# Kernel optimization log

Hardware: AMD Instinct MI355X
Metric: run time of the kernel (lower is better)

Reference implementation:

```python
import jax, jax.numpy as jnp
import numpy as np
import itertools

N_INPUTS = 6
N_TERMS = 4
# static rule index table [R, n_inputs], R = n_terms ** n_inputs = 4096
RULE_IDX = np.array(list(itertools.product(range(N_TERMS), repeat=N_INPUTS)), dtype=np.int32)


def setup_inputs() -> dict:
    key = jax.random.key(0)
    k1, k2, k3, k4 = jax.random.split(key, 4)
    B = 32768
    x = jax.random.normal(k1, (B, N_INPUTS), dtype=jnp.float32)
    centers = jax.random.normal(k2, (N_INPUTS, N_TERMS), dtype=jnp.float32)
    sigmas = jax.random.uniform(k3, (N_INPUTS, N_TERMS), dtype=jnp.float32, minval=0.5, maxval=1.5)
    consequents = jax.random.normal(k4, (N_TERMS ** N_INPUTS, N_INPUTS + 1), dtype=jnp.float32)
    return {"x": x, "centers": centers, "sigmas": sigmas, "consequents": consequents}


def reference(x, centers, sigmas, consequents):
    # Gaussian memberships: mu[b, i, t]
    s = jnp.abs(sigmas) + 1e-6                          # [I, T]
    mu = jnp.exp(-((x[:, :, None] - centers[None]) ** 2) / (2.0 * s[None] ** 2))  # [B, I, T]
    # rule firing strengths: product over inputs of selected terms
    idx = jnp.asarray(RULE_IDX.T)                       # [I, R]
    mu_sel = jnp.take_along_axis(mu, idx[None], axis=2)  # [B, I, R]
    w = jnp.prod(mu_sel, axis=1)                        # [B, R]
    w_norm = w / (jnp.sum(w, axis=1, keepdims=True) + 1e-8)
    # consequent outputs: f[b, r] = [x, 1] @ consequents[r]
    x_aug = jnp.concatenate([x, jnp.ones((x.shape[0], 1), dtype=x.dtype)], axis=1)  # [B, I+1]
    f = x_aug @ consequents.T                           # [B, R]
    return jnp.sum(w_norm * f, axis=1, keepdims=True)   # [B, 1]
```

## Files before the change

kernel.cpp:

```cpp
#include <hip/hip_runtime.h>


typedef __attribute__((ext_vector_type(8))) short bf16x8;
typedef __attribute__((ext_vector_type(4))) float f32x4;

#define THREADS 512
#define BPB     128
#define C2T_ROW_W 260
#define C2T_WORDS (64 * C2T_ROW_W)
#define PH_STR  66
#define PTT_STR 132
#define LDS_BYTES ((C2T_WORDS + BPB * PH_STR + 64 * PTT_STR) * 4)

__device__ __forceinline__ unsigned int bf16rne(float f) {
    unsigned int u = __float_as_uint(f);
    u += 0x7fffu + ((u >> 16) & 1u);
    return u >> 16;
}

__global__ void anfis_prep(const float* __restrict__ cons, unsigned int* __restrict__ ws) {
    int idx = blockIdx.x * blockDim.x + threadIdx.x;
    if (idx >= 64 * 256) return;
    int n = idx >> 8;
    int w = idx & 255;
    int c0 = w * 2;
    unsigned int h0 = 0, h1 = 0;
    int l = c0 >> 3, j = c0 & 7;
    if (j < 7) h0 = bf16rne(cons[(n * 64 + l) * 7 + j]);
    l = (c0 + 1) >> 3; j = (c0 + 1) & 7;
    if (j < 7) h1 = bf16rne(cons[(n * 64 + l) * 7 + j]);
    ws[idx] = h0 | (h1 << 16);
}

extern __shared__ unsigned int smem[];

__launch_bounds__(THREADS, 1)
__global__ void anfis_mfma(const float* __restrict__ x,
                           const float* __restrict__ centers,
                           const float* __restrict__ sigmas,
                           const unsigned int* __restrict__ wsC,
                           float* __restrict__ out, int B) {
    unsigned int* C2T = smem;
    float* PH  = (float*)(smem + C2T_WORDS);
    float* PTT = PH + BPB * PH_STR;

    const int tid  = threadIdx.x;
    const int lane = tid & 63;
    const int wv   = tid >> 6;
    const long blockbase = (long)blockIdx.x * BPB;

    for (int i = tid; i < C2T_WORDS; i += THREADS) {
        int n  = i / C2T_ROW_W;
        int ww = i - n * C2T_ROW_W;
        C2T[i] = (ww < 256) ? wsC[(n << 8) + ww] : 0u;
    }

    {
        const int d0 = (lane >> 4) & 3, d1 = (lane >> 2) & 3, d2 = lane & 3;
        float cen[6], inv[6];
        const int t6[6] = {d0, d1, d2, d0, d1, d2};
#pragma unroll
        for (int i = 0; i < 6; ++i) {
            cen[i] = centers[i * 4 + t6[i]];
            float s = fabsf(sigmas[i * 4 + t6[i]]) + 1e-6f;
            inv[i] = 0.5f / (s * s);
        }
#pragma unroll 2
        for (int g = 0; g < 16; ++g) {
            int bl = wv * 16 + g;
            long b = blockbase + bl;
            if (b >= B) b = B - 1;
            float m[6];
#pragma unroll
            for (int i = 0; i < 6; ++i) {
                float d = x[b * 6 + i] - cen[i];
                m[i] = __expf(-d * d * inv[i]);
            }
            PH[bl * PH_STR + lane]  = m[0] * m[1] * m[2];
            PTT[lane * PTT_STR + bl] = m[3] * m[4] * m[5];
        }
    }
    __syncthreads();

    const int t = lane & 15, q = lane >> 4;
    const int m0 = wv * 16;

    float xa[8];
    {
        long bm = blockbase + m0 + t;
        if (bm >= B) bm = B - 1;
#pragma unroll
        for (int j = 0; j < 6; ++j) xa[j] = x[bm * 6 + j];
        xa[6] = 1.f;
        xa[7] = 0.f;
    }

    union U4 { unsigned int u[4]; bf16x8 v; };
    U4 B4;
    B4.u[0] = B4.u[1] = B4.u[2] = 0u;
    B4.u[3] = (t == 0) ? 0x00003f80u : 0u;

    f32x4 Dn[4], D4;
#pragma unroll
    for (int nt = 0; nt < 4; ++nt) Dn[nt] = (f32x4){0.f, 0.f, 0.f, 0.f};
    D4 = (f32x4){0.f, 0.f, 0.f, 0.f};

    const unsigned short* C2Ts = (const unsigned short*)C2T;

#pragma unroll 2
    for (int kt = 0; kt < 16; ++kt) {
        float ptv = PTT[(kt * 4 + q) * PTT_STR + m0 + t];
        U4 Ah, Al;
#pragma unroll
        for (int jp = 0; jp < 4; ++jp) {
            float u0 = ptv * xa[2 * jp];
            float u1 = ptv * xa[2 * jp + 1];
            unsigned int b0 = __float_as_uint(u0), b1 = __float_as_uint(u1);
            unsigned int t0 = b0 & 0xffff0000u, t1 = b1 & 0xffff0000u;
            float l0 = u0 - __uint_as_float(t0);
            float l1 = u1 - __uint_as_float(t1);
            Ah.u[jp] = (b0 >> 16) | t1;
            Al.u[jp] = (__float_as_uint(l0) >> 16) | (__float_as_uint(l1) & 0xffff0000u);
        }
#pragma unroll
        for (int nt = 0; nt < 4; ++nt) {
            bf16x8 Bf = *(const bf16x8*)&C2Ts[(nt * 16 + t) * 520 + kt * 32 + q * 8];
            Dn[nt] = __builtin_amdgcn_mfma_f32_16x16x32_bf16(Ah.v, Bf, Dn[nt], 0, 0, 0);
            Dn[nt] = __builtin_amdgcn_mfma_f32_16x16x32_bf16(Al.v, Bf, Dn[nt], 0, 0, 0);
        }
        D4 = __builtin_amdgcn_mfma_f32_16x16x32_bf16(Ah.v, B4.v, D4, 0, 0, 0);
        D4 = __builtin_amdgcn_mfma_f32_16x16x32_bf16(Al.v, B4.v, D4, 0, 0, 0);
    }

    float Pn[4] = {0.f, 0.f, 0.f, 0.f};
    float Ps[4] = {0.f, 0.f, 0.f, 0.f};
    float Pd[4];
#pragma unroll
    for (int r = 0; r < 4; ++r) Pd[r] = D4[r];
#pragma unroll
    for (int nt = 0; nt < 4; ++nt)
#pragma unroll
        for (int r = 0; r < 4; ++r) {
            float phv = PH[(m0 + q * 4 + r) * PH_STR + nt * 16 + t];
            Pn[r] = fmaf(phv, Dn[nt][r], Pn[r]);
            Ps[r] += phv;
        }
#pragma unroll
    for (int off = 1; off < 16; off <<= 1)
#pragma unroll
        for (int r = 0; r < 4; ++r) {
            Pn[r] += __shfl_xor(Pn[r], off);
            Ps[r] += __shfl_xor(Ps[r], off);
            Pd[r] += __shfl_xor(Pd[r], off);
        }
    if (t == 0) {
        long bo = blockbase + m0 + q * 4;
        float o[4];
#pragma unroll
        for (int r = 0; r < 4; ++r) o[r] = Pn[r] / (Ps[r] * Pd[r] + 1e-8f);
        if (bo + 3 < B) {
            *(float4*)&out[bo] = make_float4(o[0], o[1], o[2], o[3]);
        } else {
#pragma unroll
            for (int r = 0; r < 4; ++r)
                if (bo + r < B) out[bo + r] = o[r];
        }
    }
}

extern "C" void kernel_launch(void* const* d_in, const int* in_sizes, int n_in,
                              void* d_out, int out_size, void* d_ws, size_t ws_size,
                              hipStream_t stream) {
    const float* x       = (const float*)d_in[0];
    const float* centers = (const float*)d_in[1];
    const float* sigmas  = (const float*)d_in[2];
    const float* cons    = (const float*)d_in[3];
    float* out = (float*)d_out;

    int B = in_sizes[0] / 6;
    unsigned int* wsC = (unsigned int*)d_ws;

    static int attr_set = 0;
    hipFuncSetAttribute(reinterpret_cast<const void*>(anfis_mfma),
                        hipFuncAttributeMaxDynamicSharedMemorySize, LDS_BYTES);
    (void)attr_set;

    anfis_prep<<<64, 256, 0, stream>>>(cons, wsC);
    int blocks = (B + BPB - 1) / BPB;
    anfis_mfma<<<blocks, THREADS, LDS_BYTES, stream>>>(x, centers, sigmas, wsC,
                                                       out, B);
}
```

Measured before the change: 80.91 us.

## Read bf16 consequents from global per wave instead of staging in LDS

The prep kernel now packs each rule's 7 consequents as one uint4 of bf16. The MFMA loop loads these packed B fragments directly from global memory, which should stay cache-resident, instead of every block first copying the whole table into LDS. Blocks shrink to 256 threads and 64 rows with 4 blocks per CU allowed. Each wave stages only its own x rows and membership partials in static shared memory, so the block-wide barrier is removed. This trades the per-block LDS fill and low occupancy for repeated global/L2 loads inside the k-loop, and it drops the tail bounds handling on x loads.

Measured after the change: 69.82 us. -13.7%, faster.

```diff
diff --git a/kernel.cpp b/kernel.cpp
--- a/kernel.cpp
+++ b/kernel.cpp
@@ -4,13 +4,10 @@
 typedef __attribute__((ext_vector_type(8))) short bf16x8;
 typedef __attribute__((ext_vector_type(4))) float f32x4;
 
-#define THREADS 512
-#define BPB     128
-#define C2T_ROW_W 260
-#define C2T_WORDS (64 * C2T_ROW_W)
+#define THREADS 256
+#define BPB     64
 #define PH_STR  66
-#define PTT_STR 132
-#define LDS_BYTES ((C2T_WORDS + BPB * PH_STR + 64 * PTT_STR) * 4)
+#define PTT_STR 65
 
 __device__ __forceinline__ unsigned int bf16rne(float f) {
     unsigned int u = __float_as_uint(f);
@@ -18,82 +15,73 @@
     return u >> 16;
 }
 
-__global__ void anfis_prep(const float* __restrict__ cons, unsigned int* __restrict__ ws) {
-    int idx = blockIdx.x * blockDim.x + threadIdx.x;
-    if (idx >= 64 * 256) return;
-    int n = idx >> 8;
-    int w = idx & 255;
-    int c0 = w * 2;
-    unsigned int h0 = 0, h1 = 0;
-    int l = c0 >> 3, j = c0 & 7;
-    if (j < 7) h0 = bf16rne(cons[(n * 64 + l) * 7 + j]);
-    l = (c0 + 1) >> 3; j = (c0 + 1) & 7;
-    if (j < 7) h1 = bf16rne(cons[(n * 64 + l) * 7 + j]);
-    ws[idx] = h0 | (h1 << 16);
+__global__ void anfis_prep(const float* __restrict__ cons, uint4* __restrict__ ws) {
+    int id = blockIdx.x * blockDim.x + threadIdx.x;
+    if (id >= 4096) return;
+    int l = id >> 6, n = id & 63;
+    const float* src = cons + (n * 64 + l) * 7;
+    unsigned int h[8];
+#pragma unroll
+    for (int j = 0; j < 7; ++j) h[j] = bf16rne(src[j]);
+    h[7] = 0;
+    uint4 v;
+    v.x = h[0] | (h[1] << 16);
+    v.y = h[2] | (h[3] << 16);
+    v.z = h[4] | (h[5] << 16);
+    v.w = h[6] | (h[7] << 16);
+    ws[id] = v;
 }
 
-extern __shared__ unsigned int smem[];
-
-__launch_bounds__(THREADS, 1)
+__launch_bounds__(THREADS, 4)
 __global__ void anfis_mfma(const float* __restrict__ x,
                            const float* __restrict__ centers,
                            const float* __restrict__ sigmas,
-                           const unsigned int* __restrict__ wsC,
+                           const uint4* __restrict__ wsC,
                            float* __restrict__ out, int B) {
-    unsigned int* C2T = smem;
-    float* PH  = (float*)(smem + C2T_WORDS);
-    float* PTT = PH + BPB * PH_STR;
+    __shared__ float  PH[BPB * PH_STR];
+    __shared__ float  PTT[64 * PTT_STR];
+    __shared__ float4 xs4[BPB * 6 / 4];
 
     const int tid  = threadIdx.x;
     const int lane = tid & 63;
     const int wv   = tid >> 6;
     const long blockbase = (long)blockIdx.x * BPB;
+    float* xs = (float*)xs4;
 
-    for (int i = tid; i < C2T_WORDS; i += THREADS) {
-        int n  = i / C2T_ROW_W;
-        int ww = i - n * C2T_ROW_W;
-        C2T[i] = (ww < 256) ? wsC[(n << 8) + ww] : 0u;
-    }
+    if (lane < 24)
+        xs4[wv * 24 + lane] = ((const float4*)x)[blockIdx.x * 96 + wv * 24 + lane];
 
     {
         const int d0 = (lane >> 4) & 3, d1 = (lane >> 2) & 3, d2 = lane & 3;
+        const int t6[6] = {d0, d1, d2, d0, d1, d2};
         float cen[6], inv[6];
-        const int t6[6] = {d0, d1, d2, d0, d1, d2};
 #pragma unroll
         for (int i = 0; i < 6; ++i) {
             cen[i] = centers[i * 4 + t6[i]];
             float s = fabsf(sigmas[i * 4 + t6[i]]) + 1e-6f;
             inv[i] = 0.5f / (s * s);
         }
-#pragma unroll 2
+#pragma unroll 4
         for (int g = 0; g < 16; ++g) {
             int bl = wv * 16 + g;
-            long b = blockbase + bl;
-            if (b >= B) b = B - 1;
             float m[6];
 #pragma unroll
             for (int i = 0; i < 6; ++i) {
-                float d = x[b * 6 + i] - cen[i];
+                float d = xs[bl * 6 + i] - cen[i];
                 m[i] = __expf(-d * d * inv[i]);
             }
-            PH[bl * PH_STR + lane]  = m[0] * m[1] * m[2];
+            PH[bl * PH_STR + lane]   = m[0] * m[1] * m[2];
             PTT[lane * PTT_STR + bl] = m[3] * m[4] * m[5];
         }
     }
-    __syncthreads();
 
-    const int t = lane & 15, q = lane >> 4;
-    const int m0 = wv * 16;
+    const int t = lane & 15, q = lane >> 4, m0 = wv * 16;
 
     float xa[8];
-    {
-        long bm = blockbase + m0 + t;
-        if (bm >= B) bm = B - 1;
 #pragma unroll
-        for (int j = 0; j < 6; ++j) xa[j] = x[bm * 6 + j];
-        xa[6] = 1.f;
-        xa[7] = 0.f;
-    }
+    for (int j = 0; j < 6; ++j) xa[j] = xs[(m0 + t) * 6 + j];
+    xa[6] = 1.f;
+    xa[7] = 0.f;
 
     union U4 { unsigned int u[4]; bf16x8 v; };
     U4 B4;
@@ -105,11 +93,17 @@
     for (int nt = 0; nt < 4; ++nt) Dn[nt] = (f32x4){0.f, 0.f, 0.f, 0.f};
     D4 = (f32x4){0.f, 0.f, 0.f, 0.f};
 
-    const unsigned short* C2Ts = (const unsigned short*)C2T;
-
 #pragma unroll 2
     for (int kt = 0; kt < 16; ++kt) {
-        float ptv = PTT[(kt * 4 + q) * PTT_STR + m0 + t];
+        const int l = kt * 4 + q;
+        U4 Bf[4];
+#pragma unroll
+        for (int nt = 0; nt < 4; ++nt) {
+            uint4 bw = wsC[l * 64 + nt * 16 + t];
+            Bf[nt].u[0] = bw.x; Bf[nt].u[1] = bw.y;
+            Bf[nt].u[2] = bw.z; Bf[nt].u[3] = bw.w;
+        }
+        float ptv = PTT[l * PTT_STR + m0 + t];
         U4 Ah, Al;
 #pragma unroll
         for (int jp = 0; jp < 4; ++jp) {
@@ -123,12 +117,12 @@
             Al.u[jp] = (__float_as_uint(l0) >> 16) | (__float_as_uint(l1) & 0xffff0000u);
         }
 #pragma unroll
-        for (int nt = 0; nt < 4; ++nt) {
-            bf16x8 Bf = *(const bf16x8*)&C2Ts[(nt * 16 + t) * 520 + kt * 32 + q * 8];
-            Dn[nt] = __builtin_amdgcn_mfma_f32_16x16x32_bf16(Ah.v, Bf, Dn[nt], 0, 0, 0);
-            Dn[nt] = __builtin_amdgcn_mfma_f32_16x16x32_bf16(Al.v, Bf, Dn[nt], 0, 0, 0);
-        }
+        for (int nt = 0; nt < 4; ++nt)
+            Dn[nt] = __builtin_amdgcn_mfma_f32_16x16x32_bf16(Ah.v, Bf[nt].v, Dn[nt], 0, 0, 0);
         D4 = __builtin_amdgcn_mfma_f32_16x16x32_bf16(Ah.v, B4.v, D4, 0, 0, 0);
+#pragma unroll
+        for (int nt = 0; nt < 4; ++nt)
+            Dn[nt] = __builtin_amdgcn_mfma_f32_16x16x32_bf16(Al.v, Bf[nt].v, Dn[nt], 0, 0, 0);
         D4 = __builtin_amdgcn_mfma_f32_16x16x32_bf16(Al.v, B4.v, D4, 0, 0, 0);
     }
 
@@ -178,15 +172,9 @@
     float* out = (float*)d_out;
 
     int B = in_sizes[0] / 6;
-    unsigned int* wsC = (unsigned int*)d_ws;
+    uint4* wsC = (uint4*)d_ws;
 
-    static int attr_set = 0;
-    hipFuncSetAttribute(reinterpret_cast<const void*>(anfis_mfma),
-                        hipFuncAttributeMaxDynamicSharedMemorySize, LDS_BYTES);
-    (void)attr_set;
-
-    anfis_prep<<<64, 256, 0, stream>>>(cons, wsC);
+    anfis_prep<<<16, 256, 0, stream>>>(cons, wsC);
     int blocks = (B + BPB - 1) / BPB;
-    anfis_mfma<<<blocks, THREADS, LDS_BYTES, stream>>>(x, centers, sigmas, wsC,
-                                                       out, B);
+    anfis_mfma<<<blocks, THREADS, 0, stream>>>(x, centers, sigmas, wsC, out, B);
 }
```
